# Performance work log

Hardware: AMD Instinct MI355X
Metric: run time of the kernel (lower is better)

Reference implementation:

```python
import jax, jax.numpy as jnp
import numpy as np

N_GENE = 100000
N_DIS = 20000
H = 128
E = 500000


def setup_inputs() -> dict:
    key = jax.random.key(0)
    ks = jax.random.split(key, 12)
    s1 = 1.0 / np.sqrt(2 * H)  # fan-in init scale, Linear(2H, H)
    s2 = 1.0 / np.sqrt(H)      # fan-in init scale, Linear(H, 1)
    z_gene = jax.random.normal(ks[0], (N_GENE, H), jnp.float32)
    z_disease = jax.random.normal(ks[1], (N_DIS, H), jnp.float32)
    # gene->disease edges: row indexes genes, col indexes diseases
    edges_gd = jnp.stack([
        jax.random.randint(ks[2], (E,), 0, N_GENE),
        jax.random.randint(ks[3], (E,), 0, N_DIS),
    ])
    # gene->gene edges
    edges_gg = jnp.stack([
        jax.random.randint(ks[4], (E,), 0, N_GENE),
        jax.random.randint(ks[5], (E,), 0, N_GENE),
    ])
    return {
        "z_gene": z_gene,
        "z_disease": z_disease,
        "edges_gd": edges_gd,
        "edges_gg": edges_gg,
        "w1_gd": jax.random.normal(ks[6], (2 * H, H), jnp.float32) * s1,
        "b1_gd": jnp.zeros((H,), jnp.float32),
        "w2_gd": jax.random.normal(ks[7], (H, 1), jnp.float32) * s2,
        "b2_gd": jnp.zeros((1,), jnp.float32),
        "w1_gg": jax.random.normal(ks[8], (2 * H, H), jnp.float32) * s1,
        "b1_gg": jnp.zeros((H,), jnp.float32),
        "w2_gg": jax.random.normal(ks[9], (H, 1), jnp.float32) * s2,
        "b2_gg": jnp.zeros((1,), jnp.float32),
    }


def _decode(z_src, z_dst, edges, w1, b1, w2, b2):
    # gather src/dst node embeddings by edge index, concat -> [E, 2H]
    z = jnp.concatenate([z_src[edges[0]], z_dst[edges[1]]], axis=1)
    h = jnp.maximum(z @ w1 + b1, 0.0)  # Linear + ReLU
    return h @ w2 + b2                  # Linear -> [E, 1]


def reference(z_gene, z_disease, edges_gd, edges_gg,
              w1_gd, b1_gd, w2_gd, b2_gd,
              w1_gg, b1_gg, w2_gg, b2_gg):
    out_gd = _decode(z_gene, z_disease, edges_gd, w1_gd, b1_gd, w2_gd, b2_gd)
    out_gg = _decode(z_gene, z_gene, edges_gg, w1_gg, b1_gg, w2_gg, b2_gg)
    # dict of per-relation outputs in the original; stack since E matches
    return jnp.stack([out_gd, out_gg])  # [2, E, 1]
```

## Files before the change

### kernel.cpp

```cpp
#include <hip/hip_runtime.h>
#include <hip/hip_bf16.h>

#define HDIM 128

typedef __attribute__((ext_vector_type(8))) short short8;
typedef __attribute__((ext_vector_type(4))) float floatx4;

__device__ __forceinline__ float bf2f(unsigned short u) {
    return __uint_as_float(((unsigned)u) << 16);
}
__device__ __forceinline__ unsigned short f2b(float f) {
    __hip_bfloat16 h = __float2bfloat16(f);
    return __builtin_bit_cast(unsigned short, h);
}
__device__ __forceinline__ float ldv(const void* p, size_t i, int flag) {
    return flag ? bf2f(((const unsigned short*)p)[i]) : ((const float*)p)[i];
}
__device__ __forceinline__ short8 pack8(float4 a, float4 b) {
    short8 r;
    r[0] = (short)f2b(a.x); r[1] = (short)f2b(a.y);
    r[2] = (short)f2b(a.z); r[3] = (short)f2b(a.w);
    r[4] = (short)f2b(b.x); r[5] = (short)f2b(b.y);
    r[6] = (short)f2b(b.z); r[7] = (short)f2b(b.w);
    return r;
}

__device__ __forceinline__ int local_detect(const unsigned short* zbits) {
    __shared__ int red[256];
    int tid = threadIdx.x;
    int cnt = 0;
    for (int i = tid; i < 4096; i += 256) {
        int ex = (zbits[i] >> 7) & 0xFF;
        if (ex >= 100 && ex <= 140) cnt++;
    }
    red[tid] = cnt;
    __syncthreads();
    for (int s = 128; s > 0; s >>= 1) {
        if (tid < s) red[tid] += red[tid + s];
        __syncthreads();
    }
    return (red[0] >= 3686) ? 1 : 0;
}

__global__ __launch_bounds__(256) void prep_kernel(
    const unsigned short* __restrict__ zbits,
    const void* __restrict__ w1_gd, const void* __restrict__ w1_gg,
    const void* __restrict__ b1_gd, const void* __restrict__ w2_gd,
    const void* __restrict__ b2_gd, const void* __restrict__ b1_gg,
    const void* __restrict__ w2_gg, const void* __restrict__ b2_gg,
    unsigned short* __restrict__ img, float* __restrict__ params,
    int* __restrict__ flagout)
{
    int flag = local_detect(zbits);
    int b = blockIdx.x;
    int tid = threadIdx.x;
    if (b < 32) {
        int im   = b >> 3;
        int sub  = b & 7;
        const void* w1 = (im < 2) ? w1_gd : w1_gg;
        int part = im & 1;
        unsigned short* out = img + im * 16384;
        int n = tid & 127;
#pragma unroll
        for (int it = 0; it < 8; ++it) {
            int k = sub * 16 + it * 2 + (tid >> 7);
            unsigned short v = flag
                ? ((const unsigned short*)w1)[(size_t)(part * 128 + k) * 128 + n]
                : f2b(((const float*)w1)[(size_t)(part * 128 + k) * 128 + n]);
            out[n * 128 + (((k >> 3) ^ (n & 15)) << 3) + (k & 7)] = v;
        }
    } else {
        if (tid < 128) {
            params[tid]       = ldv(b1_gd, tid, flag);
            params[256 + tid] = ldv(b1_gg, tid, flag);
        } else {
            params[tid]       = ldv(w2_gd, tid - 128, flag);
            params[256 + tid] = ldv(w2_gg, tid - 128, flag);
        }
        if (tid == 0) {
            params[512] = ldv(b2_gd, 0, flag);
            params[513] = ldv(b2_gg, 0, flag);
            *flagout = flag;
        }
    }
}

__global__ __launch_bounds__(256) void proj_all_kernel(
    const void* __restrict__ Zg, const void* __restrict__ Zd,
    const uint4* __restrict__ Wimg, const float* __restrict__ params,
    unsigned short* __restrict__ A_gd, unsigned short* __restrict__ B_gd,
    unsigned short* __restrict__ A_gg, unsigned short* __restrict__ B_gg,
    int NG, int ND, int gblk, const int* __restrict__ flagp)
{
    __shared__ uint4 sW[2048];
    int tid  = threadIdx.x;
    int lane = tid & 63;
    int wave = tid >> 6;
    int nl   = lane & 15;
    int quad = lane >> 4;
    int flag = *flagp;

    bool gene = (int)blockIdx.x < gblk;
    int blk = gene ? blockIdx.x : blockIdx.x - gblk;
    int M = gene ? NG : ND;
    const void* Z = gene ? Zg : Zd;

    int row0 = blk * 128 + wave * 32 + nl;
    int row1 = row0 + 16;
    int r0c = row0 < M ? row0 : (M - 1);
    int r1c = row1 < M ? row1 : (M - 1);

    short8 zf[2][4];
    if (flag) {
        const uint4* z0 = (const uint4*)Z + (size_t)r0c * 16;
        const uint4* z1 = (const uint4*)Z + (size_t)r1c * 16;
#pragma unroll
        for (int kc = 0; kc < 4; ++kc) {
            zf[0][kc] = __builtin_bit_cast(short8, z0[kc * 4 + quad]);
            zf[1][kc] = __builtin_bit_cast(short8, z1[kc * 4 + quad]);
        }
    } else {
        const float4* z0 = (const float4*)Z + (size_t)r0c * 32;
        const float4* z1 = (const float4*)Z + (size_t)r1c * 32;
#pragma unroll
        for (int kc = 0; kc < 4; ++kc) {
            int o = kc * 8 + quad * 2;
            zf[0][kc] = pack8(z0[o], z0[o + 1]);
            zf[1][kc] = pack8(z1[o], z1[o + 1]);
        }
    }

    int nph = gene ? 3 : 1;
    for (int ph = 0; ph < nph; ++ph) {
        const uint4* im;
        unsigned short* Out;
        const float* bias;
        if (gene) {
            im   = Wimg + (ph == 0 ? 0 : ph == 1 ? 2 : 3) * 2048;
            Out  = ph == 0 ? A_gd : ph == 1 ? A_gg : B_gg;
            bias = ph == 0 ? params : ph == 1 ? params + 256 : nullptr;
        } else {
            im = Wimg + 2048; Out = B_gd; bias = nullptr;
        }
        __syncthreads();
#pragma unroll
        for (int i = 0; i < 8; ++i) sW[tid + i * 256] = im[tid + i * 256];
        __syncthreads();

        floatx4 acc[2][8];
#pragma unroll
        for (int rt = 0; rt < 2; ++rt)
#pragma unroll
            for (int nt = 0; nt < 8; ++nt)
                acc[rt][nt] = (floatx4){0.f, 0.f, 0.f, 0.f};

#pragma unroll
        for (int kc = 0; kc < 4; ++kc) {
            int p = (kc * 4 + quad) ^ nl;
#pragma unroll
            for (int nt = 0; nt < 8; ++nt) {
                short8 wf = __builtin_bit_cast(short8, sW[(nt * 16 + nl) * 16 + p]);
                acc[0][nt] = __builtin_amdgcn_mfma_f32_16x16x32_bf16(wf, zf[0][kc], acc[0][nt], 0, 0, 0);
                acc[1][nt] = __builtin_amdgcn_mfma_f32_16x16x32_bf16(wf, zf[1][kc], acc[1][nt], 0, 0, 0);
            }
        }
#pragma unroll
        for (int rt = 0; rt < 2; ++rt) {
            int row = rt ? row1 : row0;
            if (row < M) {
#pragma unroll
                for (int nt = 0; nt < 8; ++nt) {
                    float4 bv = {0.f, 0.f, 0.f, 0.f};
                    if (bias) bv = *(const float4*)(bias + nt * 16 + quad * 4);
                    ushort4 v;
                    v.x = f2b(acc[rt][nt][0] + bv.x);
                    v.y = f2b(acc[rt][nt][1] + bv.y);
                    v.z = f2b(acc[rt][nt][2] + bv.z);
                    v.w = f2b(acc[rt][nt][3] + bv.w);
                    *(ushort4*)(Out + (size_t)row * HDIM + nt * 16 + quad * 4) = v;
                }
            }
        }
    }
}

__global__ __launch_bounds__(256) void edge_kernel(
    const int* __restrict__ edges_gd, const int* __restrict__ edges_gg,
    const unsigned short* __restrict__ A_gd, const unsigned short* __restrict__ B_gd,
    const unsigned short* __restrict__ A_gg, const unsigned short* __restrict__ B_gg,
    const float* __restrict__ params,
    void* __restrict__ out, int E, int nb, const int* __restrict__ flagp)
{
    int rel = ((int)blockIdx.x >= nb) ? 1 : 0;
    int blk = blockIdx.x - rel * nb;
    const int* edges = rel ? edges_gg : edges_gd;
    const unsigned short* A = rel ? A_gg : A_gd;
    const unsigned short* B = rel ? B_gg : B_gd;
    const float* w2 = params + 128 + rel * 256;
    float b2 = params[512 + rel];

    int tid  = threadIdx.x;
    int lane = tid & 63;
    int wave = tid >> 6;
    int nl   = lane & 7;
    int grp  = lane >> 3;

    float w2f[16];
#pragma unroll
    for (int i = 0; i < 4; ++i) {
        float4 t = *(const float4*)(w2 + nl * 16 + i * 4);
        w2f[i * 4 + 0] = t.x; w2f[i * 4 + 1] = t.y;
        w2f[i * 4 + 2] = t.z; w2f[i * 4 + 3] = t.w;
    }

    int e0 = blk * 64 + (wave * 8 + grp) * 2;
    int e1 = e0 + 1;
    int emax = E - 2 > 0 ? E - 2 : 0;
    int ec = e0 < emax ? e0 : emax;
    int sel = e0 - ec;
    int2 sp = *(const int2*)(edges + ec);
    int2 dp = *(const int2*)(edges + E + ec);
    int src0 = sel ? sp.y : sp.x;
    int dst0 = sel ? dp.y : dp.x;
    int src1 = sp.y;
    int dst1 = dp.y;

    const uint4* a0p = (const uint4*)(A + (size_t)src0 * HDIM) + nl * 2;
    const uint4* b0p = (const uint4*)(B + (size_t)dst0 * HDIM) + nl * 2;
    const uint4* a1p = (const uint4*)(A + (size_t)src1 * HDIM) + nl * 2;
    const uint4* b1p = (const uint4*)(B + (size_t)dst1 * HDIM) + nl * 2;
    uint4 a0[2] = {a0p[0], a0p[1]};
    uint4 c0[2] = {b0p[0], b0p[1]};
    uint4 a1[2] = {a1p[0], a1p[1]};
    uint4 c1[2] = {b1p[0], b1p[1]};

    float acc0 = 0.f, acc1 = 0.f;
#pragma unroll
    for (int i = 0; i < 2; ++i) {
        const unsigned* au0 = (const unsigned*)&a0[i];
        const unsigned* cu0 = (const unsigned*)&c0[i];
        const unsigned* au1 = (const unsigned*)&a1[i];
        const unsigned* cu1 = (const unsigned*)&c1[i];
#pragma unroll
        for (int j = 0; j < 4; ++j) {
            int ch = i * 8 + j * 2;
            float x0 = __uint_as_float(au0[j] << 16);
            float x1 = __uint_as_float(au0[j] & 0xffff0000u);
            float y0 = __uint_as_float(cu0[j] << 16);
            float y1 = __uint_as_float(cu0[j] & 0xffff0000u);
            acc0 = fmaf(fmaxf(x0 + y0, 0.f), w2f[ch], acc0);
            acc0 = fmaf(fmaxf(x1 + y1, 0.f), w2f[ch + 1], acc0);
            float u0 = __uint_as_float(au1[j] << 16);
            float u1 = __uint_as_float(au1[j] & 0xffff0000u);
            float v0 = __uint_as_float(cu1[j] << 16);
            float v1 = __uint_as_float(cu1[j] & 0xffff0000u);
            acc1 = fmaf(fmaxf(u0 + v0, 0.f), w2f[ch], acc1);
            acc1 = fmaf(fmaxf(u1 + v1, 0.f), w2f[ch + 1], acc1);
        }
    }
    acc0 += __shfl_xor(acc0, 1); acc1 += __shfl_xor(acc1, 1);
    acc0 += __shfl_xor(acc0, 2); acc1 += __shfl_xor(acc1, 2);
    acc0 += __shfl_xor(acc0, 4); acc1 += __shfl_xor(acc1, 4);

    if (nl == 0) {
        int flag = *flagp;
        size_t base = (size_t)rel * E;
        if (e0 < E) {
            float r = acc0 + b2;
            if (flag) ((unsigned short*)out)[base + e0] = f2b(r);
            else      ((float*)out)[base + e0] = r;
        }
        if (e1 < E) {
            float r = acc1 + b2;
            if (flag) ((unsigned short*)out)[base + e1] = f2b(r);
            else      ((float*)out)[base + e1] = r;
        }
    }
}

__global__ __launch_bounds__(256) void detect_kernel(
    const unsigned short* __restrict__ zbits, int* __restrict__ flag)
{
    int f = local_detect(zbits);
    if (threadIdx.x == 0) *flag = f;
}

__global__ __launch_bounds__(128) void naive_edge_kernel(
    const int* __restrict__ edges,
    const void* __restrict__ zsrc, const void* __restrict__ zdst,
    const void* __restrict__ w1, const void* __restrict__ b1,
    const void* __restrict__ w2, const void* __restrict__ b2,
    void* __restrict__ out, size_t eoff, int E,
    const int* __restrict__ flagp)
{
    int flag = flagp ? *flagp : 0;
    __shared__ float zs[128], zd[128], red[128];
    int e = blockIdx.x;
    int n = threadIdx.x;
    int src = edges[e], dst = edges[E + e];
    zs[n] = ldv(zsrc, (size_t)src * HDIM + n, flag);
    zd[n] = ldv(zdst, (size_t)dst * HDIM + n, flag);
    __syncthreads();
    float acc = ldv(b1, n, flag);
    for (int k = 0; k < 128; ++k) acc = fmaf(zs[k], ldv(w1, (size_t)k * HDIM + n, flag), acc);
    for (int k = 0; k < 128; ++k) acc = fmaf(zd[k], ldv(w1, (size_t)(128 + k) * HDIM + n, flag), acc);
    red[n] = fmaxf(acc, 0.f) * ldv(w2, n, flag);
    __syncthreads();
    for (int s = 64; s > 0; s >>= 1) {
        if (n < s) red[n] += red[n + s];
        __syncthreads();
    }
    if (n == 0) {
        float r = red[0] + ldv(b2, 0, flag);
        if (flag) ((unsigned short*)out)[eoff + e] = f2b(r);
        else      ((float*)out)[eoff + e] = r;
    }
}

extern "C" void kernel_launch(void* const* d_in, const int* in_sizes, int n_in,
                              void* d_out, int out_size, void* d_ws, size_t ws_size,
                              hipStream_t stream)
{
    const void* z_gene = d_in[0];
    const void* z_dis  = d_in[1];
    const int* edges_gd = (const int*)d_in[2];
    const int* edges_gg = (const int*)d_in[3];
    const void* w1_gd = d_in[4];
    const void* b1_gd = d_in[5];
    const void* w2_gd = d_in[6];
    const void* b2_gd = d_in[7];
    const void* w1_gg = d_in[8];
    const void* b1_gg = d_in[9];
    const void* w2_gg = d_in[10];
    const void* b2_gg = d_in[11];

    int NG = in_sizes[0] / HDIM;
    int ND = in_sizes[1] / HDIM;
    int E  = in_sizes[2] / 2;

    size_t off_flag   = 0;
    size_t off_params = 256;
    size_t off_img    = 2560;
    size_t off_Agd    = off_img + 131072;
    size_t off_Bgd    = off_Agd + (size_t)NG * HDIM * 2;
    size_t off_Agg    = off_Bgd + (size_t)ND * HDIM * 2;
    size_t off_Bgg    = off_Agg + (size_t)NG * HDIM * 2;
    size_t need       = off_Bgg + (size_t)NG * HDIM * 2;

    char* ws = (char*)d_ws;

    if (ws_size < need) {
        const int* flagp = nullptr;
        if (ws_size >= 16) {
            detect_kernel<<<1, 256, 0, stream>>>((const unsigned short*)z_gene, (int*)ws);
            flagp = (const int*)ws;
        }
        naive_edge_kernel<<<E, 128, 0, stream>>>(edges_gd, z_gene, z_dis,
                                                 w1_gd, b1_gd, w2_gd, b2_gd,
                                                 d_out, 0, E, flagp);
        naive_edge_kernel<<<E, 128, 0, stream>>>(edges_gg, z_gene, z_gene,
                                                 w1_gg, b1_gg, w2_gg, b2_gg,
                                                 d_out, (size_t)E, E, flagp);
        return;
    }

    int* flag = (int*)(ws + off_flag);
    float* params = (float*)(ws + off_params);
    unsigned short* img = (unsigned short*)(ws + off_img);
    unsigned short* Agd = (unsigned short*)(ws + off_Agd);
    unsigned short* Bgd = (unsigned short*)(ws + off_Bgd);
    unsigned short* Agg = (unsigned short*)(ws + off_Agg);
    unsigned short* Bgg = (unsigned short*)(ws + off_Bgg);

    prep_kernel<<<33, 256, 0, stream>>>((const unsigned short*)z_gene,
                                        w1_gd, w1_gg, b1_gd, w2_gd, b2_gd,
                                        b1_gg, w2_gg, b2_gg, img, params, flag);

    const uint4* img4 = (const uint4*)img;
    int gblk = (NG + 127) / 128;
    int dblk = (ND + 127) / 128;
    proj_all_kernel<<<gblk + dblk, 256, 0, stream>>>(z_gene, z_dis, img4, params,
                                                     Agd, Bgd, Agg, Bgg,
                                                     NG, ND, gblk, flag);

    int nb = (E + 63) / 64;
    edge_kernel<<<2 * nb, 256, 0, stream>>>(edges_gd, edges_gg, Agd, Bgd, Agg, Bgg,
                                            params, d_out, E, nb, flag);
}
```

Before: 225.4 us.

## Split projection phases across blocks and process four edges per lane group

The projection kernel no longer loops over three weight phases inside each gene block. Each phase now gets its own blocks (3*gblk+dblk), so the work spreads over more CUs with one weight load and one barrier per block, at the cost of reloading the Z rows three times. The edge kernel now handles four edges per 8-lane group, using int4 edge-index loads and vectorized float4/ushort4 output stores when E is a multiple of 4. This raises the number of gathers in flight and halves the block count.

```diff
diff --git a/kernel.cpp b/kernel.cpp
--- a/kernel.cpp
+++ b/kernel.cpp
@@ -100,10 +100,18 @@
     int quad = lane >> 4;
     int flag = *flagp;
 
-    bool gene = (int)blockIdx.x < gblk;
-    int blk = gene ? blockIdx.x : blockIdx.x - gblk;
+    int b  = blockIdx.x;
+    int ph = (b >= gblk) + (b >= 2 * gblk) + (b >= 3 * gblk);
+    bool gene = ph < 3;
+    int blk = b - ph * gblk;
     int M = gene ? NG : ND;
     const void* Z = gene ? Zg : Zd;
+    const uint4* im = Wimg + (ph == 0 ? 0 : ph == 1 ? 2 : ph == 2 ? 3 : 1) * 2048;
+    unsigned short* Out = ph == 0 ? A_gd : ph == 1 ? A_gg : ph == 2 ? B_gg : B_gd;
+    const float* bias = ph == 0 ? params : ph == 1 ? params + 256 : nullptr;
+
+#pragma unroll
+    for (int i = 0; i < 8; ++i) sW[tid + i * 256] = im[tid + i * 256];
 
     int row0 = blk * 128 + wave * 32 + nl;
     int row1 = row0 + 16;
@@ -130,55 +138,39 @@
         }
     }
 
-    int nph = gene ? 3 : 1;
-    for (int ph = 0; ph < nph; ++ph) {
-        const uint4* im;
-        unsigned short* Out;
-        const float* bias;
-        if (gene) {
-            im   = Wimg + (ph == 0 ? 0 : ph == 1 ? 2 : 3) * 2048;
-            Out  = ph == 0 ? A_gd : ph == 1 ? A_gg : B_gg;
-            bias = ph == 0 ? params : ph == 1 ? params + 256 : nullptr;
-        } else {
-            im = Wimg + 2048; Out = B_gd; bias = nullptr;
-        }
-        __syncthreads();
-#pragma unroll
-        for (int i = 0; i < 8; ++i) sW[tid + i * 256] = im[tid + i * 256];
-        __syncthreads();
-
-        floatx4 acc[2][8];
-#pragma unroll
-        for (int rt = 0; rt < 2; ++rt)
-#pragma unroll
-            for (int nt = 0; nt < 8; ++nt)
-                acc[rt][nt] = (floatx4){0.f, 0.f, 0.f, 0.f};
-
-#pragma unroll
-        for (int kc = 0; kc < 4; ++kc) {
-            int p = (kc * 4 + quad) ^ nl;
+    __syncthreads();
+
+    floatx4 acc[2][8];
+#pragma unroll
+    for (int rt = 0; rt < 2; ++rt)
+#pragma unroll
+        for (int nt = 0; nt < 8; ++nt)
+            acc[rt][nt] = (floatx4){0.f, 0.f, 0.f, 0.f};
+
+#pragma unroll
+    for (int kc = 0; kc < 4; ++kc) {
+        int p = (kc * 4 + quad) ^ nl;
+#pragma unroll
+        for (int nt = 0; nt < 8; ++nt) {
+            short8 wf = __builtin_bit_cast(short8, sW[(nt * 16 + nl) * 16 + p]);
+            acc[0][nt] = __builtin_amdgcn_mfma_f32_16x16x32_bf16(wf, zf[0][kc], acc[0][nt], 0, 0, 0);
+            acc[1][nt] = __builtin_amdgcn_mfma_f32_16x16x32_bf16(wf, zf[1][kc], acc[1][nt], 0, 0, 0);
+        }
+    }
+#pragma unroll
+    for (int rt = 0; rt < 2; ++rt) {
+        int row = rt ? row1 : row0;
+        if (row < M) {
 #pragma unroll
             for (int nt = 0; nt < 8; ++nt) {
-                short8 wf = __builtin_bit_cast(short8, sW[(nt * 16 + nl) * 16 + p]);
-                acc[0][nt] = __builtin_amdgcn_mfma_f32_16x16x32_bf16(wf, zf[0][kc], acc[0][nt], 0, 0, 0);
-                acc[1][nt] = __builtin_amdgcn_mfma_f32_16x16x32_bf16(wf, zf[1][kc], acc[1][nt], 0, 0, 0);
-            }
-        }
-#pragma unroll
-        for (int rt = 0; rt < 2; ++rt) {
-            int row = rt ? row1 : row0;
-            if (row < M) {
-#pragma unroll
-                for (int nt = 0; nt < 8; ++nt) {
-                    float4 bv = {0.f, 0.f, 0.f, 0.f};
-                    if (bias) bv = *(const float4*)(bias + nt * 16 + quad * 4);
-                    ushort4 v;
-                    v.x = f2b(acc[rt][nt][0] + bv.x);
-                    v.y = f2b(acc[rt][nt][1] + bv.y);
-                    v.z = f2b(acc[rt][nt][2] + bv.z);
-                    v.w = f2b(acc[rt][nt][3] + bv.w);
-                    *(ushort4*)(Out + (size_t)row * HDIM + nt * 16 + quad * 4) = v;
-                }
+                float4 bv = {0.f, 0.f, 0.f, 0.f};
+                if (bias) bv = *(const float4*)(bias + nt * 16 + quad * 4);
+                ushort4 v;
+                v.x = f2b(acc[rt][nt][0] + bv.x);
+                v.y = f2b(acc[rt][nt][1] + bv.y);
+                v.z = f2b(acc[rt][nt][2] + bv.z);
+                v.w = f2b(acc[rt][nt][3] + bv.w);
+                *(ushort4*)(Out + (size_t)row * HDIM + nt * 16 + quad * 4) = v;
             }
         }
     }
@@ -213,67 +205,83 @@
         w2f[i * 4 + 2] = t.z; w2f[i * 4 + 3] = t.w;
     }
 
-    int e0 = blk * 64 + (wave * 8 + grp) * 2;
-    int e1 = e0 + 1;
-    int emax = E - 2 > 0 ? E - 2 : 0;
-    int ec = e0 < emax ? e0 : emax;
-    int sel = e0 - ec;
-    int2 sp = *(const int2*)(edges + ec);
-    int2 dp = *(const int2*)(edges + E + ec);
-    int src0 = sel ? sp.y : sp.x;
-    int dst0 = sel ? dp.y : dp.x;
-    int src1 = sp.y;
-    int dst1 = dp.y;
-
-    const uint4* a0p = (const uint4*)(A + (size_t)src0 * HDIM) + nl * 2;
-    const uint4* b0p = (const uint4*)(B + (size_t)dst0 * HDIM) + nl * 2;
-    const uint4* a1p = (const uint4*)(A + (size_t)src1 * HDIM) + nl * 2;
-    const uint4* b1p = (const uint4*)(B + (size_t)dst1 * HDIM) + nl * 2;
-    uint4 a0[2] = {a0p[0], a0p[1]};
-    uint4 c0[2] = {b0p[0], b0p[1]};
-    uint4 a1[2] = {a1p[0], a1p[1]};
-    uint4 c1[2] = {b1p[0], b1p[1]};
-
-    float acc0 = 0.f, acc1 = 0.f;
-#pragma unroll
-    for (int i = 0; i < 2; ++i) {
-        const unsigned* au0 = (const unsigned*)&a0[i];
-        const unsigned* cu0 = (const unsigned*)&c0[i];
-        const unsigned* au1 = (const unsigned*)&a1[i];
-        const unsigned* cu1 = (const unsigned*)&c1[i];
-#pragma unroll
-        for (int j = 0; j < 4; ++j) {
-            int ch = i * 8 + j * 2;
-            float x0 = __uint_as_float(au0[j] << 16);
-            float x1 = __uint_as_float(au0[j] & 0xffff0000u);
-            float y0 = __uint_as_float(cu0[j] << 16);
-            float y1 = __uint_as_float(cu0[j] & 0xffff0000u);
-            acc0 = fmaf(fmaxf(x0 + y0, 0.f), w2f[ch], acc0);
-            acc0 = fmaf(fmaxf(x1 + y1, 0.f), w2f[ch + 1], acc0);
-            float u0 = __uint_as_float(au1[j] << 16);
-            float u1 = __uint_as_float(au1[j] & 0xffff0000u);
-            float v0 = __uint_as_float(cu1[j] << 16);
-            float v1 = __uint_as_float(cu1[j] & 0xffff0000u);
-            acc1 = fmaf(fmaxf(u0 + v0, 0.f), w2f[ch], acc1);
-            acc1 = fmaf(fmaxf(u1 + v1, 0.f), w2f[ch + 1], acc1);
-        }
-    }
-    acc0 += __shfl_xor(acc0, 1); acc1 += __shfl_xor(acc1, 1);
-    acc0 += __shfl_xor(acc0, 2); acc1 += __shfl_xor(acc1, 2);
-    acc0 += __shfl_xor(acc0, 4); acc1 += __shfl_xor(acc1, 4);
+    int e0 = blk * 128 + (wave * 8 + grp) * 4;
+    bool al = (E & 3) == 0;
+    int ebase = e0;
+    int src[4], dst[4];
+    if (al) {
+        ebase = e0 <= E - 4 ? e0 : E - 4;
+        int4 s4 = *(const int4*)(edges + ebase);
+        int4 d4 = *(const int4*)(edges + E + ebase);
+        src[0] = s4.x; src[1] = s4.y; src[2] = s4.z; src[3] = s4.w;
+        dst[0] = d4.x; dst[1] = d4.y; dst[2] = d4.z; dst[3] = d4.w;
+    } else {
+#pragma unroll
+        for (int i = 0; i < 4; ++i) {
+            int e = e0 + i; e = e < E ? e : E - 1;
+            src[i] = edges[e]; dst[i] = edges[E + e];
+        }
+    }
+
+    uint4 av[4][2], bv[4][2];
+#pragma unroll
+    for (int i = 0; i < 4; ++i) {
+        const uint4* ap = (const uint4*)(A + (size_t)src[i] * HDIM) + nl * 2;
+        const uint4* bp = (const uint4*)(B + (size_t)dst[i] * HDIM) + nl * 2;
+        av[i][0] = ap[0]; av[i][1] = ap[1];
+        bv[i][0] = bp[0]; bv[i][1] = bp[1];
+    }
+
+    float acc[4] = {0.f, 0.f, 0.f, 0.f};
+#pragma unroll
+    for (int i = 0; i < 4; ++i) {
+#pragma unroll
+        for (int h = 0; h < 2; ++h) {
+            const unsigned* au = (const unsigned*)&av[i][h];
+            const unsigned* bu = (const unsigned*)&bv[i][h];
+#pragma unroll
+            for (int j = 0; j < 4; ++j) {
+                int ch = h * 8 + j * 2;
+                float x0 = __uint_as_float(au[j] << 16);
+                float x1 = __uint_as_float(au[j] & 0xffff0000u);
+                float y0 = __uint_as_float(bu[j] << 16);
+                float y1 = __uint_as_float(bu[j] & 0xffff0000u);
+                acc[i] = fmaf(fmaxf(x0 + y0, 0.f), w2f[ch], acc[i]);
+                acc[i] = fmaf(fmaxf(x1 + y1, 0.f), w2f[ch + 1], acc[i]);
+            }
+        }
+    }
+#pragma unroll
+    for (int i = 0; i < 4; ++i) {
+        acc[i] += __shfl_xor(acc[i], 1);
+        acc[i] += __shfl_xor(acc[i], 2);
+        acc[i] += __shfl_xor(acc[i], 4);
+    }
 
     if (nl == 0) {
         int flag = *flagp;
         size_t base = (size_t)rel * E;
-        if (e0 < E) {
-            float r = acc0 + b2;
-            if (flag) ((unsigned short*)out)[base + e0] = f2b(r);
-            else      ((float*)out)[base + e0] = r;
-        }
-        if (e1 < E) {
-            float r = acc1 + b2;
-            if (flag) ((unsigned short*)out)[base + e1] = f2b(r);
-            else      ((float*)out)[base + e1] = r;
+        if (al) {
+            if (flag) {
+                ushort4 v;
+                v.x = f2b(acc[0] + b2); v.y = f2b(acc[1] + b2);
+                v.z = f2b(acc[2] + b2); v.w = f2b(acc[3] + b2);
+                *(ushort4*)((unsigned short*)out + base + ebase) = v;
+            } else {
+                float4 v;
+                v.x = acc[0] + b2; v.y = acc[1] + b2;
+                v.z = acc[2] + b2; v.w = acc[3] + b2;
+                *(float4*)((float*)out + base + ebase) = v;
+            }
+        } else {
+#pragma unroll
+            for (int i = 0; i < 4; ++i) {
+                if (e0 + i < E) {
+                    float r = acc[i] + b2;
+                    if (flag) ((unsigned short*)out)[base + e0 + i] = f2b(r);
+                    else      ((float*)out)[base + e0 + i] = r;
+                }
+            }
         }
     }
 }
@@ -379,11 +387,11 @@
     const uint4* img4 = (const uint4*)img;
     int gblk = (NG + 127) / 128;
     int dblk = (ND + 127) / 128;
-    proj_all_kernel<<<gblk + dblk, 256, 0, stream>>>(z_gene, z_dis, img4, params,
-                                                     Agd, Bgd, Agg, Bgg,
-                                                     NG, ND, gblk, flag);
-
-    int nb = (E + 63) / 64;
+    proj_all_kernel<<<3 * gblk + dblk, 256, 0, stream>>>(z_gene, z_dis, img4, params,
+                                                         Agd, Bgd, Agg, Bgg,
+                                                         NG, ND, gblk, flag);
+
+    int nb = (E + 127) / 128;
     edge_kernel<<<2 * nb, 256, 0, stream>>>(edges_gd, edges_gg, Agd, Bgd, Agg, Bgg,
                                             params, d_out, E, nb, flag);
 }
```

New measurement: 226.3 us. No clear change (+0.4%).

## Split gene projection phases across blocks and stage output stores through LDS

Applied to the files above, without the earlier changes.

Each gene block used to loop over three weight phases. Now every (phase, row-block) pair gets its own block, which triples the gene grid and removes the serial loop and the repeated weight reload inside a block. The output tile is staged through padded shared memory so each row is written to global memory as coalesced 16-byte stores instead of scattered 8-byte ones. In exchange, each gene row's embeddings are read from global memory three times instead of once, and extra barriers are added.

```diff
diff --git a/kernel.cpp b/kernel.cpp
--- a/kernel.cpp
+++ b/kernel.cpp
@@ -100,10 +100,18 @@
     int quad = lane >> 4;
     int flag = *flagp;
 
-    bool gene = (int)blockIdx.x < gblk;
-    int blk = gene ? blockIdx.x : blockIdx.x - gblk;
+    int b  = blockIdx.x;
+    int ph = (b >= gblk) + (b >= 2 * gblk) + (b >= 3 * gblk);
+    bool gene = ph < 3;
+    int blk = b - ph * gblk;
     int M = gene ? NG : ND;
     const void* Z = gene ? Zg : Zd;
+    const uint4* im = Wimg + (ph == 0 ? 0 : ph == 1 ? 2 : ph == 2 ? 3 : 1) * 2048;
+    unsigned short* Out = ph == 0 ? A_gd : ph == 1 ? A_gg : ph == 2 ? B_gg : B_gd;
+    const float* bias = ph == 0 ? params : ph == 1 ? params + 256 : nullptr;
+
+#pragma unroll
+    for (int i = 0; i < 8; ++i) sW[tid + i * 256] = im[tid + i * 256];
 
     int row0 = blk * 128 + wave * 32 + nl;
     int row1 = row0 + 16;
@@ -130,57 +138,51 @@
         }
     }
 
-    int nph = gene ? 3 : 1;
-    for (int ph = 0; ph < nph; ++ph) {
-        const uint4* im;
-        unsigned short* Out;
-        const float* bias;
-        if (gene) {
-            im   = Wimg + (ph == 0 ? 0 : ph == 1 ? 2 : 3) * 2048;
-            Out  = ph == 0 ? A_gd : ph == 1 ? A_gg : B_gg;
-            bias = ph == 0 ? params : ph == 1 ? params + 256 : nullptr;
-        } else {
-            im = Wimg + 2048; Out = B_gd; bias = nullptr;
+    __syncthreads();
+
+    floatx4 acc[2][8];
+#pragma unroll
+    for (int rt = 0; rt < 2; ++rt)
+#pragma unroll
+        for (int nt = 0; nt < 8; ++nt)
+            acc[rt][nt] = (floatx4){0.f, 0.f, 0.f, 0.f};
+
+#pragma unroll
+    for (int kc = 0; kc < 4; ++kc) {
+        int p = (kc * 4 + quad) ^ nl;
+#pragma unroll
+        for (int nt = 0; nt < 8; ++nt) {
+            short8 wf = __builtin_bit_cast(short8, sW[(nt * 16 + nl) * 16 + p]);
+            acc[0][nt] = __builtin_amdgcn_mfma_f32_16x16x32_bf16(wf, zf[0][kc], acc[0][nt], 0, 0, 0);
+            acc[1][nt] = __builtin_amdgcn_mfma_f32_16x16x32_bf16(wf, zf[1][kc], acc[1][nt], 0, 0, 0);
+        }
+    }
+
+    char* sOb = (char*)sW;
+    __syncthreads();
+#pragma unroll
+    for (int rt = 0; rt < 2; ++rt) {
+        int h = wave * 16 + nl;
+#pragma unroll
+        for (int nt = 0; nt < 8; ++nt) {
+            float4 bv = {0.f, 0.f, 0.f, 0.f};
+            if (bias) bv = *(const float4*)(bias + nt * 16 + quad * 4);
+            unsigned lo = ((unsigned)f2b(acc[rt][nt][0] + bv.x)) |
+                          (((unsigned)f2b(acc[rt][nt][1] + bv.y)) << 16);
+            unsigned hi = ((unsigned)f2b(acc[rt][nt][2] + bv.z)) |
+                          (((unsigned)f2b(acc[rt][nt][3] + bv.w)) << 16);
+            uint2 v; v.x = lo; v.y = hi;
+            *(uint2*)(sOb + h * 264 + nt * 32 + quad * 8) = v;
         }
         __syncthreads();
 #pragma unroll
-        for (int i = 0; i < 8; ++i) sW[tid + i * 256] = im[tid + i * 256];
-        __syncthreads();
-
-        floatx4 acc[2][8];
-#pragma unroll
-        for (int rt = 0; rt < 2; ++rt)
-#pragma unroll
-            for (int nt = 0; nt < 8; ++nt)
-                acc[rt][nt] = (floatx4){0.f, 0.f, 0.f, 0.f};
-
-#pragma unroll
-        for (int kc = 0; kc < 4; ++kc) {
-            int p = (kc * 4 + quad) ^ nl;
-#pragma unroll
-            for (int nt = 0; nt < 8; ++nt) {
-                short8 wf = __builtin_bit_cast(short8, sW[(nt * 16 + nl) * 16 + p]);
-                acc[0][nt] = __builtin_amdgcn_mfma_f32_16x16x32_bf16(wf, zf[0][kc], acc[0][nt], 0, 0, 0);
-                acc[1][nt] = __builtin_amdgcn_mfma_f32_16x16x32_bf16(wf, zf[1][kc], acc[1][nt], 0, 0, 0);
-            }
-        }
-#pragma unroll
-        for (int rt = 0; rt < 2; ++rt) {
-            int row = rt ? row1 : row0;
-            if (row < M) {
-#pragma unroll
-                for (int nt = 0; nt < 8; ++nt) {
-                    float4 bv = {0.f, 0.f, 0.f, 0.f};
-                    if (bias) bv = *(const float4*)(bias + nt * 16 + quad * 4);
-                    ushort4 v;
-                    v.x = f2b(acc[rt][nt][0] + bv.x);
-                    v.y = f2b(acc[rt][nt][1] + bv.y);
-                    v.z = f2b(acc[rt][nt][2] + bv.z);
-                    v.w = f2b(acc[rt][nt][3] + bv.w);
-                    *(ushort4*)(Out + (size_t)row * HDIM + nt * 16 + quad * 4) = v;
-                }
-            }
-        }
+        for (int j = 0; j < 4; ++j) {
+            int r = blk * 128 + rt * 16 + j * 32 + (tid >> 4);
+            uint4 v = *(const uint4*)(sOb + (j * 16 + (tid >> 4)) * 264 + (tid & 15) * 16);
+            if (r < M)
+                *(uint4*)(Out + (size_t)r * HDIM + (tid & 15) * 8) = v;
+        }
+        if (rt == 0) __syncthreads();
     }
 }
 
@@ -379,9 +381,9 @@
     const uint4* img4 = (const uint4*)img;
     int gblk = (NG + 127) / 128;
     int dblk = (ND + 127) / 128;
-    proj_all_kernel<<<gblk + dblk, 256, 0, stream>>>(z_gene, z_dis, img4, params,
-                                                     Agd, Bgd, Agg, Bgg,
-                                                     NG, ND, gblk, flag);
+    proj_all_kernel<<<3 * gblk + dblk, 256, 0, stream>>>(z_gene, z_dis, img4, params,
+                                                         Agd, Bgd, Agg, Bgg,
+                                                         NG, ND, gblk, flag);
 
     int nb = (E + 63) / 64;
     edge_kernel<<<2 * nb, 256, 0, stream>>>(edges_gd, edges_gg, Agd, Bgd, Agg, Bgg,
```

New measurement: 223.8 us. Within noise of the previous version (-0.7%).
